# Performance work log

Hardware: AMD Instinct MI355X
Metric: run time of the kernel (lower is better)

## Reference

```python
import jax, jax.numpy as jnp
import numpy as np

N = 100000        # num nodes
E2 = 3200000      # num directed edges (symmetric)
D = 256           # node feature dim
C = 40            # num classes
NIDS = 1000       # labelled node ids
TOL = 0.01
MAXITER = 16
AVG_DEG = E2 // N // 2 * 2  # ~32


def setup_inputs() -> dict:
    key = jax.random.key(0)
    k1, k2, k3, k4, k5, k6 = jax.random.split(key, 6)
    E = E2 // 2
    row_h = jax.random.randint(k1, (E,), 0, N, dtype=jnp.int32)
    col_h = jax.random.randint(k2, (E,), 0, N, dtype=jnp.int32)
    # symmetrize so I - (1-eps)*A is SPD-like (CG assumption)
    row = jnp.concatenate([row_h, col_h])
    col = jnp.concatenate([col_h, row_h])
    vals = jax.random.uniform(k3, (E,), dtype=jnp.float32) * (0.9 / 32.0)
    data = jnp.concatenate([vals, vals])
    node_features = jax.random.normal(k4, (N, D), dtype=jnp.float32)
    ids = jax.random.randint(k5, (NIDS,), 0, N, dtype=jnp.int32)
    # hk.Linear with TruncatedNormal(stddev=1/sqrt(D)) init
    W = (jax.random.truncated_normal(k6, -2.0, 2.0, (D, C), dtype=jnp.float32)
         * (1.0 / np.sqrt(D))).astype(jnp.float32)
    b = jnp.zeros((C,), jnp.float32)
    e0 = jnp.zeros((), jnp.float32)  # hk.get_parameter('e0', (), init=zeros)
    return dict(node_features=node_features, W=W, b=b, e0=e0,
                data=data, row=row, col=col, ids=ids)


def reference(node_features, W, b, e0, data, row, col, ids):
    epsilon = jax.nn.sigmoid(e0)
    # head_transform=None; d_feat > num_classes -> Linear first, then smooth
    x = node_features @ W + b  # [N, C]

    def spmv(v):  # adj @ v for COO adjacency, v: [N, C]
        return jax.ops.segment_sum(data[:, None] * v[col], row, num_segments=N)

    def f(v):  # (I - (1-eps) A) v
        return v - (1.0 - epsilon) * spmv(v)

    # smooth(): x.shape[1] (=C) <= ids.size -> direct CG on dense x, then gather ids
    sol, _ = jax.scipy.sparse.linalg.cg(f, x, tol=TOL, maxiter=MAXITER)
    return sol[ids]  # [NIDS, C] logits
```

## Files before the change

kernel.cpp:

```cpp
#include <hip/hip_runtime.h>
#include <hip/hip_fp16.h>
#include <math.h>

#define NNODE  100000
#define NEDGE  3200000
#define DFEAT  256
#define NCLS   40
#define NC_TOT 4000000
#define NIDS   1000
#define TOLSQ  1.0e-4f
#define MAXIT  16

#define SB 2048
#define SLOT8 500000
#define SPB8 245
#define XB 1024
#define VT 256
#define GR     128
#define GKC    32
#define GEMM_B 782

#define RB      128
#define NBUCK   782
#define BCAP    6144
#define SUBB    1024
#define NPB     800
#define EPB     4000

__device__ __forceinline__ float block_reduce_256(float v, float* red) {
  int tid = threadIdx.x;
  red[tid] = v;
  __syncthreads();
  #pragma unroll
  for (int off = 128; off > 0; off >>= 1) {
    if (tid < off) red[tid] += red[tid + off];
    __syncthreads();
  }
  float res = red[0];
  __syncthreads();
  return res;
}

__global__ void __launch_bounds__(256) k_pcount(const int* __restrict__ row,
                                                int* __restrict__ cntmat,
                                                int* __restrict__ total) {
  __shared__ int h[NBUCK];
  int tid = threadIdx.x, blk = blockIdx.x;
  for (int i = tid; i < NBUCK; i += 256) h[i] = 0;
  __syncthreads();
  int e0 = blk * EPB;
  for (int i = tid; i < EPB; i += 256) atomicAdd(&h[row[e0 + i] >> 7], 1);
  __syncthreads();
  for (int i = tid; i < NBUCK; i += 256) {
    int v = h[i];
    cntmat[blk * NBUCK + i] = v;
    if (v) atomicAdd(&total[i], v);
  }
}

__global__ void k_bscan2(const int* __restrict__ total, int* __restrict__ bptr) {
  __shared__ int s[1024];
  int tid = threadIdx.x;
  int v = (tid < NBUCK) ? total[tid] : 0;
  s[tid] = v;
  __syncthreads();
  for (int off = 1; off < 1024; off <<= 1) {
    int t = (tid >= off) ? s[tid - off] : 0;
    __syncthreads();
    s[tid] += t;
    __syncthreads();
  }
  if (tid < NBUCK) bptr[tid] = s[tid] - v;
  if (tid == 0) bptr[NBUCK] = NEDGE;
}

__global__ void __launch_bounds__(1024) k_colscan(int* __restrict__ cntmat,
                                                  const int* __restrict__ bptr) {
  __shared__ int s[1024];
  int b = blockIdx.x;
  int tid = threadIdx.x;
  int v = (tid < NPB) ? cntmat[tid * NBUCK + b] : 0;
  s[tid] = v;
  __syncthreads();
  for (int off = 1; off < 1024; off <<= 1) {
    int t = (tid >= off) ? s[tid - off] : 0;
    __syncthreads();
    s[tid] += t;
    __syncthreads();
  }
  if (tid < NPB) cntmat[tid * NBUCK + b] = bptr[b] + s[tid] - v;
}

__global__ void __launch_bounds__(512) k_ppart(const int* __restrict__ row,
    const int* __restrict__ col, const float* __restrict__ data,
    const int* __restrict__ offmat, uint2* __restrict__ bstage) {
  __shared__ int cnt[NBUCK];
  __shared__ int segs[NBUCK + 1];
  __shared__ int cur[NBUCK];
  __shared__ int goff[NBUCK];
  __shared__ int scp[512];
  __shared__ unsigned short bof[EPB];
  __shared__ uint2 pay[EPB];
  int tid = threadIdx.x, blk = blockIdx.x;
  int e0 = blk * EPB;

  for (int i = tid; i < NBUCK; i += 512) {
    cnt[i] = 0;
    goff[i] = offmat[blk * NBUCK + i];
  }
  __syncthreads();
  for (int i = tid; i < EPB; i += 512) atomicAdd(&cnt[row[e0 + i] >> 7], 1);
  __syncthreads();

  int t2 = tid * 2;
  int l0 = (t2 + 0 < NBUCK) ? cnt[t2 + 0] : 0;
  int l1 = (t2 + 1 < NBUCK) ? cnt[t2 + 1] : 0;
  int mysum = l0 + l1;
  scp[tid] = mysum;
  __syncthreads();
  for (int off = 1; off < 512; off <<= 1) {
    int t = (tid >= off) ? scp[tid - off] : 0;
    __syncthreads();
    scp[tid] += t;
    __syncthreads();
  }
  int base = scp[tid] - mysum;
  if (t2 + 0 <= NBUCK) segs[t2 + 0] = base;  base += l0;
  if (t2 + 1 <= NBUCK) segs[t2 + 1] = base;
  for (int i = tid; i < NBUCK; i += 512) cur[i] = 0;
  __syncthreads();

  for (int b = tid; b < NBUCK; b += 512) {
    int s1 = segs[b + 1];
    for (int i = segs[b]; i < s1; ++i) bof[i] = (unsigned short)b;
  }
  for (int i = tid; i < EPB; i += 512) {
    int rr = row[e0 + i];
    int b = rr >> 7;
    int rk = atomicAdd(&cur[b], 1);
    pay[segs[b] + rk] = make_uint2(((unsigned)(rr & (RB - 1)) << 17) | (unsigned)col[e0 + i],
                                   __float_as_uint(data[e0 + i]));
  }
  __syncthreads();
  for (int i = tid; i < EPB; i += 512) {
    int b = bof[i];
    bstage[goff[b] + (i - segs[b])] = pay[i];
  }
}

__global__ void __launch_bounds__(512) k_bbuild(const int* __restrict__ bptr,
    const uint2* __restrict__ bstage, int* __restrict__ rowptr,
    int2* __restrict__ csr) {
  __shared__ uint2 ebuf[BCAP];
  __shared__ int deg[SUBB];
  __shared__ int segs[SUBB];
  __shared__ int scp[512];
  int b = blockIdx.x;
  int s0 = bptr[b], s1 = bptr[b + 1];
  int n = s1 - s0;
  if (n > BCAP) n = BCAP;
  int tid = threadIdx.x;
  for (int i = tid; i < SUBB; i += 512) deg[i] = 0;
  __syncthreads();
  for (int i = tid; i < n; i += 512) {
    uint2 e = bstage[s0 + i];
    ebuf[i] = e;
    int key = (int)(e.x >> 17) * 8 + (int)((e.x & 0x1FFFF) >> 14);
    atomicAdd(&deg[key], 1);
  }
  __syncthreads();
  int t2 = tid * 2;
  int l0 = deg[t2 + 0], l1 = deg[t2 + 1];
  int mysum = l0 + l1;
  scp[tid] = mysum;
  __syncthreads();
  for (int off = 1; off < 512; off <<= 1) {
    int t = (tid >= off) ? scp[tid - off] : 0;
    __syncthreads();
    scp[tid] += t;
    __syncthreads();
  }
  int base = scp[tid] - mysum;
  segs[t2 + 0] = base;  base += l0;
  segs[t2 + 1] = base;
  __syncthreads();
  for (int i = tid; i < SUBB; i += 512) deg[i] = 0;
  if (tid < RB) {
    int grow = b * RB + tid;
    if (grow < NNODE) rowptr[grow] = s0 + segs[tid * 8];
  }
  if (b == 0 && tid == 0) rowptr[NNODE] = NEDGE;
  __syncthreads();
  for (int i = tid; i < n; i += 512) {
    uint2 e = ebuf[i];
    int col = (int)(e.x & 0x1FFFF);
    int key = (int)(e.x >> 17) * 8 + (col >> 14);
    int pos = atomicAdd(&deg[key], 1);
    csr[s0 + segs[key] + pos] = make_int2(col, (int)e.y);
  }
}

__global__ void __launch_bounds__(256) k_gemm(const float* __restrict__ feat,
    const float* __restrict__ W, const float* __restrict__ bias,
    float* __restrict__ r, float* __restrict__ p, __half* __restrict__ ph,
    float* __restrict__ part) {
  __shared__ float ftile[2][GR][GKC + 1];
  __shared__ float wtile[2][GKC * NCLS];
  __shared__ float red[256];
  int tid = threadIdx.x;
  int r0 = blockIdx.x * GR;
  int rl0 = (tid >> 2) * 2;
  int cbase = (tid & 3) * 10;
  float acc0[10], acc1[10];
  #pragma unroll
  for (int j = 0; j < 10; ++j) {
    float bv = bias[cbase + j];
    acc0[j] = bv;
    acc1[j] = bv;
  }

  float4 sf[4];
  float sw[5];
  int srr[4], skq[4];
  #pragma unroll
  for (int it = 0; it < 4; ++it) {
    int i = tid + it * 256;
    srr[it] = i >> 3;
    skq[it] = i & 7;
  }

  #pragma unroll
  for (int it = 0; it < 4; ++it) {
    int grow = r0 + srr[it];
    sf[it] = make_float4(0.f, 0.f, 0.f, 0.f);
    if (grow < NNODE)
      sf[it] = *(const float4*)(feat + (size_t)grow * DFEAT + skq[it] * 4);
  }
  #pragma unroll
  for (int it = 0; it < 5; ++it) sw[it] = W[tid + it * 256];
  #pragma unroll
  for (int it = 0; it < 4; ++it) {
    ftile[0][srr[it]][skq[it] * 4 + 0] = sf[it].x;
    ftile[0][srr[it]][skq[it] * 4 + 1] = sf[it].y;
    ftile[0][srr[it]][skq[it] * 4 + 2] = sf[it].z;
    ftile[0][srr[it]][skq[it] * 4 + 3] = sf[it].w;
  }
  #pragma unroll
  for (int it = 0; it < 5; ++it) wtile[0][tid + it * 256] = sw[it];
  __syncthreads();

  for (int t = 0; t < DFEAT / GKC; ++t) {
    if (t + 1 < DFEAT / GKC) {
      int k0n = (t + 1) * GKC;
      #pragma unroll
      for (int it = 0; it < 4; ++it) {
        int grow = r0 + srr[it];
        sf[it] = make_float4(0.f, 0.f, 0.f, 0.f);
        if (grow < NNODE)
          sf[it] = *(const float4*)(feat + (size_t)grow * DFEAT + k0n + skq[it] * 4);
      }
      #pragma unroll
      for (int it = 0; it < 5; ++it) sw[it] = W[k0n * NCLS + tid + it * 256];
    }
    int buf = t & 1;
    #pragma unroll 4
    for (int kk = 0; kk < GKC; ++kk) {
      float f0 = ftile[buf][rl0][kk];
      float f1 = ftile[buf][rl0 + 1][kk];
      const float* wr = &wtile[buf][kk * NCLS + cbase];
      #pragma unroll
      for (int j = 0; j < 10; ++j) {
        float w = wr[j];
        acc0[j] = fmaf(f0, w, acc0[j]);
        acc1[j] = fmaf(f1, w, acc1[j]);
      }
    }
    if (t + 1 < DFEAT / GKC) {
      int nb = (t + 1) & 1;
      #pragma unroll
      for (int it = 0; it < 4; ++it) {
        ftile[nb][srr[it]][skq[it] * 4 + 0] = sf[it].x;
        ftile[nb][srr[it]][skq[it] * 4 + 1] = sf[it].y;
        ftile[nb][srr[it]][skq[it] * 4 + 2] = sf[it].z;
        ftile[nb][srr[it]][skq[it] * 4 + 3] = sf[it].w;
      }
      #pragma unroll
      for (int it = 0; it < 5; ++it) wtile[nb][tid + it * 256] = sw[it];
      __syncthreads();
    }
  }

  float local = 0.f;
  int g0 = r0 + rl0, g1 = g0 + 1;
  if (g0 < NNODE) {
    size_t b0 = (size_t)g0 * NCLS + cbase;
    #pragma unroll
    for (int j = 0; j < 10; ++j) {
      float a = acc0[j];
      r[b0 + j] = a; p[b0 + j] = a; ph[b0 + j] = __float2half(a);
      local = fmaf(a, a, local);
    }
  }
  if (g1 < NNODE) {
    size_t b1 = (size_t)g1 * NCLS + cbase;
    #pragma unroll
    for (int j = 0; j < 10; ++j) {
      float a = acc1[j];
      r[b1 + j] = a; p[b1 + j] = a; ph[b1 + j] = __float2half(a);
      local = fmaf(a, a, local);
    }
  }
  float tot = block_reduce_256(local, red);
  if (tid == 0) part[blockIdx.x] = tot;
}

__global__ void k_init_scal(const float* __restrict__ part, const float* __restrict__ e0,
                            float* __restrict__ scal) {
  __shared__ float red[256];
  float local = 0.f;
  for (int i = threadIdx.x; i < GEMM_B; i += 256) local += part[i];
  float bs = block_reduce_256(local, red);
  if (threadIdx.x == 0) {
    float eps = 1.f / (1.f + expf(-e0[0]));
    scal[0] = 1.f - eps;
    scal[1] = TOLSQ * bs;
    scal[2] = bs;
  }
}

__global__ void __launch_bounds__(VT) k_spmv(const float* __restrict__ scal, int k,
    const int* __restrict__ rowptr, const int2* __restrict__ csr,
    const __half* __restrict__ ph, const float* __restrict__ p,
    float* __restrict__ Ap, float* __restrict__ part) {
  float gamma = scal[2 + k], atol2 = scal[1];
  if (!(gamma > atol2)) return;
  float omega = scal[0];
  int b = blockIdx.x;
  int chunk = (b & 7) * (SB / 8) + (b >> 3);
  int sbase = chunk * SPB8;
  float local = 0.f;
  int li = threadIdx.x;
  int s = sbase + li;
  if (li < SPB8 && s < SLOT8) {
    int rr = s / 5;
    int c8 = (s - rr * 5) * 8;
    int s0 = rowptr[rr], s1 = rowptr[rr + 1];
    float a0 = 0.f, a1 = 0.f, a2 = 0.f, a3 = 0.f;
    float a4 = 0.f, a5 = 0.f, a6 = 0.f, a7 = 0.f;
    #pragma unroll 4
    for (int j = s0; j < s1; ++j) {
      int2 pr = csr[j];
      float w = __int_as_float(pr.y);
      uint4 g = *(const uint4*)(ph + (size_t)pr.x * NCLS + c8);
      float2 f01 = __half22float2(*(__half2*)&g.x);
      float2 f23 = __half22float2(*(__half2*)&g.y);
      float2 f45 = __half22float2(*(__half2*)&g.z);
      float2 f67 = __half22float2(*(__half2*)&g.w);
      a0 = fmaf(w, f01.x, a0); a1 = fmaf(w, f01.y, a1);
      a2 = fmaf(w, f23.x, a2); a3 = fmaf(w, f23.y, a3);
      a4 = fmaf(w, f45.x, a4); a5 = fmaf(w, f45.y, a5);
      a6 = fmaf(w, f67.x, a6); a7 = fmaf(w, f67.y, a7);
    }
    size_t e = (size_t)rr * NCLS + c8;
    float4 pe0 = *(const float4*)(p + e);
    float4 pe1 = *(const float4*)(p + e + 4);
    float4 v0, v1;
    v0.x = fmaf(-omega, a0, pe0.x); v0.y = fmaf(-omega, a1, pe0.y);
    v0.z = fmaf(-omega, a2, pe0.z); v0.w = fmaf(-omega, a3, pe0.w);
    v1.x = fmaf(-omega, a4, pe1.x); v1.y = fmaf(-omega, a5, pe1.y);
    v1.z = fmaf(-omega, a6, pe1.z); v1.w = fmaf(-omega, a7, pe1.w);
    *(float4*)(Ap + e) = v0;
    *(float4*)(Ap + e + 4) = v1;
    local = fmaf(pe0.x, v0.x, local); local = fmaf(pe0.y, v0.y, local);
    local = fmaf(pe0.z, v0.z, local); local = fmaf(pe0.w, v0.w, local);
    local = fmaf(pe1.x, v1.x, local); local = fmaf(pe1.y, v1.y, local);
    local = fmaf(pe1.z, v1.z, local); local = fmaf(pe1.w, v1.w, local);
  }
  __shared__ float red[256];
  float tot = block_reduce_256(local, red);
  if (threadIdx.x == 0) part[blockIdx.x] = tot;
}

__global__ void __launch_bounds__(VT) k_xr(const float* __restrict__ scal, int k,
    const float* __restrict__ part_in,
    const float* __restrict__ p, const float* __restrict__ Ap,
    float* __restrict__ r, const int* __restrict__ ids,
    float* __restrict__ out, float* __restrict__ part_out) {
  float gamma = scal[2 + k], atol2 = scal[1];
  if (!(gamma > atol2)) return;
  __shared__ float red[256];
  float lp = 0.f;
  for (int i = threadIdx.x; i < SB; i += VT) lp += part_in[i];
  float pap = block_reduce_256(lp, red);
  float alpha = gamma / pap;
  int idx = blockIdx.x * VT + threadIdx.x;
  if (idx < NIDS * NCLS) {
    int i = idx / NCLS, c = idx - (idx / NCLS) * NCLS;
    out[idx] += alpha * p[(size_t)ids[i] * NCLS + c];
  }
  const float4* a4 = (const float4*)Ap;
  float4* r4 = (float4*)r;
  float local = 0.f;
  int stride = gridDim.x * blockDim.x;
  for (int e = blockIdx.x * blockDim.x + threadIdx.x; e < NC_TOT / 4; e += stride) {
    float4 ae = a4[e], re = r4[e];
    re.x = fmaf(-alpha, ae.x, re.x); re.y = fmaf(-alpha, ae.y, re.y);
    re.z = fmaf(-alpha, ae.z, re.z); re.w = fmaf(-alpha, ae.w, re.w);
    r4[e] = re;
    local = fmaf(re.x, re.x, local); local = fmaf(re.y, re.y, local);
    local = fmaf(re.z, re.z, local); local = fmaf(re.w, re.w, local);
  }
  float tot = block_reduce_256(local, red);
  if (threadIdx.x == 0) part_out[blockIdx.x] = tot;
}

__global__ void __launch_bounds__(VT) k_pupd(float* __restrict__ scal, int k,
    const float* __restrict__ part_in,
    const float* __restrict__ r, float* __restrict__ p, __half* __restrict__ ph) {
  float gamma = scal[2 + k], atol2 = scal[1];
  if (!(gamma > atol2)) {
    if (blockIdx.x == 0 && threadIdx.x == 0) scal[2 + k + 1] = gamma;
    return;
  }
  __shared__ float red[256];
  float lp = 0.f;
  for (int i = threadIdx.x; i < XB; i += VT) lp += part_in[i];
  float gnew = block_reduce_256(lp, red);
  float beta = gnew / gamma;
  const float4* r4 = (const float4*)r;
  float4* p4 = (float4*)p;
  int stride = gridDim.x * blockDim.x;
  for (int e = blockIdx.x * blockDim.x + threadIdx.x; e < NC_TOT / 4; e += stride) {
    float4 pe = p4[e], re = r4[e];
    pe.x = fmaf(beta, pe.x, re.x); pe.y = fmaf(beta, pe.y, re.y);
    pe.z = fmaf(beta, pe.z, re.z); pe.w = fmaf(beta, pe.w, re.w);
    p4[e] = pe;
    int e4 = e * 4;
    ph[e4 + 0] = __float2half(pe.x);
    ph[e4 + 1] = __float2half(pe.y);
    ph[e4 + 2] = __float2half(pe.z);
    ph[e4 + 3] = __float2half(pe.w);
  }
  if (blockIdx.x == 0 && threadIdx.x == 0) scal[2 + k + 1] = gnew;
}

extern "C" void kernel_launch(void* const* d_in, const int* in_sizes, int n_in,
                              void* d_out, int out_size, void* d_ws, size_t ws_size,
                              hipStream_t stream) {
  const float* feat = (const float*)d_in[0];
  const float* W    = (const float*)d_in[1];
  const float* bias = (const float*)d_in[2];
  const float* e0   = (const float*)d_in[3];
  const float* data = (const float*)d_in[4];
  const int*   row  = (const int*)d_in[5];
  const int*   col  = (const int*)d_in[6];
  const int*   ids  = (const int*)d_in[7];
  float* out = (float*)d_out;

  size_t off = 0;
  char* base = (char*)d_ws;
  auto take = [&](size_t nbytes) -> void* {
    void* ptr = base + off;
    off += (nbytes + 255) & ~(size_t)255;
    return ptr;
  };
  float* rv  = (float*)take((size_t)NC_TOT * 4);
  float* pv  = (float*)take((size_t)NC_TOT * 4);
  float* ap  = (float*)take((size_t)NC_TOT * 4);
  __half* ph = (__half*)take((size_t)NC_TOT * 2);
  int2*  csr = (int2*)take((size_t)NEDGE * 8);
  int* rowptr    = (int*)take((size_t)(NNODE + 1) * 4);
  int* cntmat    = (int*)take((size_t)NPB * NBUCK * 4);
  int* total     = (int*)take((size_t)(NBUCK + 2) * 4);
  int* bptr      = (int*)take((size_t)(NBUCK + 2) * 4);
  float* part_a  = (float*)take(SB * 4);
  float* part_b  = (float*)take(XB * 4);
  float* scal    = (float*)take(64 * 4);

  uint2* bstage = (uint2*)rv;

  hipMemsetAsync(total, 0, (size_t)(NBUCK + 2) * 4, stream);
  hipMemsetAsync(out, 0, (size_t)NIDS * NCLS * 4, stream);
  k_pcount<<<NPB, 256, 0, stream>>>(row, cntmat, total);
  k_bscan2<<<1, 1024, 0, stream>>>(total, bptr);
  k_colscan<<<NBUCK, 1024, 0, stream>>>(cntmat, bptr);
  k_ppart<<<NPB, 512, 0, stream>>>(row, col, data, cntmat, bstage);
  k_bbuild<<<NBUCK, 512, 0, stream>>>(bptr, bstage, rowptr, csr);

  k_gemm<<<GEMM_B, 256, 0, stream>>>(feat, W, bias, rv, pv, ph, part_a);
  k_init_scal<<<1, 256, 0, stream>>>(part_a, e0, scal);

  for (int k = 0; k < MAXIT; ++k) {
    k_spmv<<<SB, VT, 0, stream>>>(scal, k, rowptr, csr, ph, pv, ap, part_a);
    k_xr  <<<XB, VT, 0, stream>>>(scal, k, part_a, pv, ap, rv, ids, out, part_b);
    k_pupd<<<XB, VT, 0, stream>>>(scal, k, part_b, rv, pv, ph);
  }
}
```

Before: 393.4 us.

## Load full W into shared memory and stream features directly from global

The GEMM kernel no longer double-buffers feature and weight tiles through shared memory. It now loads the whole 256x40 weight matrix into LDS once per block. Each thread then reads its two feature rows straight from global memory with float4 loads, which removes the per-tile barriers and LDS staging. The cost is about 40KB of LDS per block, which may lower occupancy, and uncoalesced per-thread row reads that depend on the cache for efficiency.

```diff
diff --git a/kernel.cpp b/kernel.cpp
--- a/kernel.cpp
+++ b/kernel.cpp
@@ -17,7 +17,6 @@
 #define XB 1024
 #define VT 256
 #define GR     128
-#define GKC    32
 #define GEMM_B 782
 
 #define RB      128
@@ -204,8 +203,7 @@
     const float* __restrict__ W, const float* __restrict__ bias,
     float* __restrict__ r, float* __restrict__ p, __half* __restrict__ ph,
     float* __restrict__ part) {
-  __shared__ float ftile[2][GR][GKC + 1];
-  __shared__ float wtile[2][GKC * NCLS];
+  __shared__ float wtile[DFEAT * NCLS];
   __shared__ float red[256];
   int tid = threadIdx.x;
   int r0 = blockIdx.x * GR;
@@ -219,79 +217,40 @@
     acc1[j] = bv;
   }
 
-  float4 sf[4];
-  float sw[5];
-  int srr[4], skq[4];
   #pragma unroll
-  for (int it = 0; it < 4; ++it) {
-    int i = tid + it * 256;
-    srr[it] = i >> 3;
-    skq[it] = i & 7;
-  }
-
-  #pragma unroll
-  for (int it = 0; it < 4; ++it) {
-    int grow = r0 + srr[it];
-    sf[it] = make_float4(0.f, 0.f, 0.f, 0.f);
-    if (grow < NNODE)
-      sf[it] = *(const float4*)(feat + (size_t)grow * DFEAT + skq[it] * 4);
-  }
-  #pragma unroll
-  for (int it = 0; it < 5; ++it) sw[it] = W[tid + it * 256];
-  #pragma unroll
-  for (int it = 0; it < 4; ++it) {
-    ftile[0][srr[it]][skq[it] * 4 + 0] = sf[it].x;
-    ftile[0][srr[it]][skq[it] * 4 + 1] = sf[it].y;
-    ftile[0][srr[it]][skq[it] * 4 + 2] = sf[it].z;
-    ftile[0][srr[it]][skq[it] * 4 + 3] = sf[it].w;
-  }
-  #pragma unroll
-  for (int it = 0; it < 5; ++it) wtile[0][tid + it * 256] = sw[it];
-  __syncthreads();
-
-  for (int t = 0; t < DFEAT / GKC; ++t) {
-    if (t + 1 < DFEAT / GKC) {
-      int k0n = (t + 1) * GKC;
-      #pragma unroll
-      for (int it = 0; it < 4; ++it) {
-        int grow = r0 + srr[it];
-        sf[it] = make_float4(0.f, 0.f, 0.f, 0.f);
-        if (grow < NNODE)
-          sf[it] = *(const float4*)(feat + (size_t)grow * DFEAT + k0n + skq[it] * 4);
-      }
-      #pragma unroll
-      for (int it = 0; it < 5; ++it) sw[it] = W[k0n * NCLS + tid + it * 256];
+  for (int it = 0; it < DFEAT * NCLS / 256; ++it)
+    wtile[tid + it * 256] = W[tid + it * 256];
+  __syncthreads();
+
+  int g0 = r0 + rl0, g1 = g0 + 1;
+  int g0c = (g0 < NNODE) ? g0 : NNODE - 1;
+  int g1c = (g1 < NNODE) ? g1 : NNODE - 1;
+  const float* f0p = feat + (size_t)g0c * DFEAT;
+  const float* f1p = feat + (size_t)g1c * DFEAT;
+
+  #pragma unroll 4
+  for (int kq = 0; kq < DFEAT / 4; ++kq) {
+    float4 f0 = *(const float4*)(f0p + kq * 4);
+    float4 f1 = *(const float4*)(f1p + kq * 4);
+    const float* w0 = &wtile[(kq * 4 + 0) * NCLS + cbase];
+    const float* w1 = &wtile[(kq * 4 + 1) * NCLS + cbase];
+    const float* w2 = &wtile[(kq * 4 + 2) * NCLS + cbase];
+    const float* w3 = &wtile[(kq * 4 + 3) * NCLS + cbase];
+    #pragma unroll
+    for (int j = 0; j < 10; ++j) {
+      float wa = w0[j], wb = w1[j], wc = w2[j], wd = w3[j];
+      acc0[j] = fmaf(f0.x, wa, acc0[j]);
+      acc0[j] = fmaf(f0.y, wb, acc0[j]);
+      acc0[j] = fmaf(f0.z, wc, acc0[j]);
+      acc0[j] = fmaf(f0.w, wd, acc0[j]);
+      acc1[j] = fmaf(f1.x, wa, acc1[j]);
+      acc1[j] = fmaf(f1.y, wb, acc1[j]);
+      acc1[j] = fmaf(f1.z, wc, acc1[j]);
+      acc1[j] = fmaf(f1.w, wd, acc1[j]);
     }
-    int buf = t & 1;
-    #pragma unroll 4
-    for (int kk = 0; kk < GKC; ++kk) {
-      float f0 = ftile[buf][rl0][kk];
-      float f1 = ftile[buf][rl0 + 1][kk];
-      const float* wr = &wtile[buf][kk * NCLS + cbase];
-      #pragma unroll
-      for (int j = 0; j < 10; ++j) {
-        float w = wr[j];
-        acc0[j] = fmaf(f0, w, acc0[j]);
-        acc1[j] = fmaf(f1, w, acc1[j]);
-      }
-    }
-    if (t + 1 < DFEAT / GKC) {
-      int nb = (t + 1) & 1;
-      #pragma unroll
-      for (int it = 0; it < 4; ++it) {
-        ftile[nb][srr[it]][skq[it] * 4 + 0] = sf[it].x;
-        ftile[nb][srr[it]][skq[it] * 4 + 1] = sf[it].y;
-        ftile[nb][srr[it]][skq[it] * 4 + 2] = sf[it].z;
-        ftile[nb][srr[it]][skq[it] * 4 + 3] = sf[it].w;
-      }
-      #pragma unroll
-      for (int it = 0; it < 5; ++it) wtile[nb][tid + it * 256] = sw[it];
-      __syncthreads();
-    }
   }
 
   float local = 0.f;
-  int g0 = r0 + rl0, g1 = g0 + 1;
   if (g0 < NNODE) {
     size_t b0 = (size_t)g0 * NCLS + cbase;
     #pragma unroll
```

Measured after the change: 389.7 us (median of 2 runs). No clear change (-0.9%).
